# Performance work log

Hardware: AMD Instinct MI355X
Metric: run time of the kernel (lower is better)

The kernel has to match this reference:

```python
import jax, jax.numpy as jnp
import numpy as np

B, K, F, HID, NCLS = 32, 32, 2048, 2, 47
BN_EPS = 1e-5


def setup_inputs() -> dict:
    key = jax.random.key(0)
    ks = jax.random.split(key, 12)
    x = jax.random.normal(ks[0], (B, 1, F), dtype=jnp.float32)
    neighbor = jax.random.normal(ks[1], (B, K, 1, F), dtype=jnp.float32)
    # FeatBrd1d conv1d kernel_size=1 weights: (out_ch, in_ch)
    w1 = jax.random.normal(ks[2], (HID, 1), dtype=jnp.float32) * 0.5
    b1 = jax.random.normal(ks[3], (HID,), dtype=jnp.float32) * 0.1
    g1 = jnp.ones((HID,), dtype=jnp.float32)
    beta1 = jnp.zeros((HID,), dtype=jnp.float32)
    w2 = jax.random.normal(ks[4], (HID, HID), dtype=jnp.float32) * 0.5
    b2 = jax.random.normal(ks[5], (HID,), dtype=jnp.float32) * 0.1
    g2 = jnp.ones((HID,), dtype=jnp.float32)
    beta2 = jnp.zeros((HID,), dtype=jnp.float32)
    Wc = jax.random.normal(ks[6], (NCLS, HID * F), dtype=jnp.float32) * (1.0 / np.sqrt(HID * F))
    bc = jnp.zeros((NCLS,), dtype=jnp.float32)
    return {"x": x, "neighbor": neighbor, "w1": w1, "b1": b1, "g1": g1,
            "beta1": beta1, "w2": w2, "b2": b2, "g2": g2, "beta2": beta2,
            "Wc": Wc, "bc": bc}


def feature_adjacency(x, neighbor):
    # fadj[b] = sum_{k} x[b,0,:] outer neighbor[b,k,0,:]  -> (B, F, F)
    ysum = neighbor.sum(axis=(1, 2))                      # (B, F)
    fadj = jnp.einsum('bf,bg->bfg', x[:, 0, :], ysum)
    fadj = fadj + jnp.swapaxes(fadj, -2, -1)
    # sgnroot
    fadj = jnp.sign(fadj) * jnp.sqrt(jnp.abs(fadj))
    # row_normalize (torch sums over dim=1 of (B,F,F))
    denom = jnp.abs(fadj).sum(axis=1, keepdims=True) + 1e-7
    fadj = fadj / denom
    return jnp.nan_to_num(fadj, nan=0.0, posinf=None, neginf=None)


def featbrd(x, fadj, w, b):
    # conv1d kernel-size-1: (B, Cin, F) x (Cout, Cin) -> (B, Cout, F)
    h = jnp.einsum('bif,oi->bof', x, w) + b[None, :, None]
    # adj broadcast: out[b,c,f] = sum_g fadj[b,f,g] * h[b,c,g]
    return jnp.einsum('bfg,bcg->bcf', fadj, h)


def bn_softsign(x, gamma, beta):
    # BatchNorm1d training mode over (B, C, F): stats per channel over (B, F)
    mean = x.mean(axis=(0, 2), keepdims=True)
    var = ((x - mean) ** 2).mean(axis=(0, 2), keepdims=True)
    xn = (x - mean) * jax.lax.rsqrt(var + BN_EPS)
    y = gamma[None, :, None] * xn + beta[None, :, None]
    return y / (1.0 + jnp.abs(y))  # Softsign


def reference(x, neighbor, w1, b1, g1, beta1, w2, b2, g2, beta2, Wc, bc):
    fadj = feature_adjacency(x, neighbor)
    h = bn_softsign(featbrd(x, fadj, w1, b1), g1, beta1)
    h = bn_softsign(featbrd(h, fadj, w2, b2), g2, beta2)
    flat = h.reshape(h.shape[0], -1)                      # (B, HID*F)
    return flat @ Wc.T + bc
```

## Files before the change

kernel.cpp:

```cpp
#include <hip/hip_runtime.h>
#include <math.h>

namespace {

constexpr int Bn   = 32;
constexpr int Kn   = 32;
constexpr int Fn   = 2048;
constexpr int HIDn = 2;
constexpr int NCLSn = 47;
constexpr float EPSn = 1e-5f;
constexpr int NT = 256;
constexpr int GS = 16;
constexpr int FT = Fn / GS;

typedef float v2f __attribute__((ext_vector_type(2)));
typedef float v4f __attribute__((ext_vector_type(4)));

__device__ inline float wave_sum(float v) {
    #pragma unroll
    for (int off = 32; off > 0; off >>= 1) v += __shfl_down(v, off, 64);
    return v;
}

__global__ void ysum_kernel(const float* __restrict__ neighbor,
                            float* __restrict__ ysum,
                            double* __restrict__ stats) {
    int idx4 = blockIdx.x * NT + threadIdx.x;
    if (blockIdx.x == 0 && threadIdx.x < 8) stats[threadIdx.x] = 0.0;
    int b = idx4 >> 9;
    int gq = idx4 & 511;
    const float* p = neighbor + (size_t)b * Kn * Fn + gq * 4;
    v4f s = (v4f){0.f, 0.f, 0.f, 0.f};
    #pragma unroll
    for (int k = 0; k < Kn; ++k) s += *(const v4f*)(p + (size_t)k * Fn);
    *(v4f*)(ysum + (size_t)b * Fn + gq * 4) = s;
}

__global__ __launch_bounds__(NT, 4)
void denom_partial_kernel(const float* __restrict__ x, const float* __restrict__ ysum,
                          float* __restrict__ dpart) {
    __shared__ v4f xyf4[FT];
    const int gtile = blockIdx.x;
    const int fs    = blockIdx.y;
    const int b     = blockIdx.z;
    const int tid   = threadIdx.x;
    const float* xb = x + (size_t)b * Fn;
    const float* yb = ysum + (size_t)b * Fn;
    if (tid < FT) {
        int f = fs * FT + tid;
        float xv = xb[f], yv = yb[f];
        xyf4[tid] = (v4f){xv, xv, yv, yv};
    }
    const int gbase = (gtile * NT + tid) * 4;
    const v4f Xg4 = *(const v4f*)(xb + gbase);
    const v4f Yg4 = *(const v4f*)(yb + gbase);
    const v2f Xg01 = (v2f){Xg4.x, Xg4.y}, Xg23 = (v2f){Xg4.z, Xg4.w};
    const v2f Yg01 = (v2f){Yg4.x, Yg4.y}, Yg23 = (v2f){Yg4.z, Yg4.w};
    __syncthreads();
    v2f d01 = (v2f){0.f, 0.f}, d23 = (v2f){0.f, 0.f};
    #pragma unroll 8
    for (int j = 0; j < FT; ++j) {
        v4f q = xyf4[j];
        v2f xf = (v2f){q.x, q.y}, yf = (v2f){q.z, q.w};
        v2f vA = Xg01 * yf + Yg01 * xf;
        v2f vB = Xg23 * yf + Yg23 * xf;
        v2f sA, sB;
        sA.x = __builtin_amdgcn_sqrtf(fabsf(vA.x));
        sA.y = __builtin_amdgcn_sqrtf(fabsf(vA.y));
        sB.x = __builtin_amdgcn_sqrtf(fabsf(vB.x));
        sB.y = __builtin_amdgcn_sqrtf(fabsf(vB.y));
        d01 += sA;
        d23 += sB;
    }
    v4f dout = (v4f){d01.x, d01.y, d23.x, d23.y};
    *(v4f*)(dpart + ((size_t)fs * Bn + b) * Fn + gbase) = dout;
}

__device__ inline void mv_loop4(const v4f* __restrict__ xy4, const v4f* __restrict__ tt4,
                                v2f Xf01, v2f Xf23, v2f Yf01, v2f Yf23,
                                v2f& a00, v2f& a10, v2f& a01, v2f& a11) {
    #pragma unroll 8
    for (int j = 0; j < FT; ++j) {
        v4f q = xy4[j];
        v2f xg = (v2f){q.x, q.y}, yg = (v2f){q.z, q.w};
        v2f vA = Xf01 * yg + Yf01 * xg;
        v2f vB = Xf23 * yg + Yf23 * xg;
        v2f SA, SB;
        SA.x = copysignf(__builtin_amdgcn_sqrtf(fabsf(vA.x)), vA.x);
        SA.y = copysignf(__builtin_amdgcn_sqrtf(fabsf(vA.y)), vA.y);
        SB.x = copysignf(__builtin_amdgcn_sqrtf(fabsf(vB.x)), vB.x);
        SB.y = copysignf(__builtin_amdgcn_sqrtf(fabsf(vB.y)), vB.y);
        v4f u = tt4[j];
        v2f t0 = (v2f){u.x, u.y}, t1 = (v2f){u.z, u.w};
        a00 += SA * t0;
        a10 += SA * t1;
        a01 += SB * t0;
        a11 += SB * t1;
    }
}

__global__ __launch_bounds__(NT, 4)
void mv1_partial_kernel(const float* __restrict__ x, const float* __restrict__ ysum,
                        const float* __restrict__ dpart,
                        const float* __restrict__ w1, const float* __restrict__ b1,
                        float* __restrict__ part) {
    __shared__ v4f xy4[FT], tt4[FT];
    const int ftile = blockIdx.x;
    const int gs    = blockIdx.y;
    const int b     = blockIdx.z;
    const int tid   = threadIdx.x;
    const float* xb = x + (size_t)b * Fn;
    const float* yb = ysum + (size_t)b * Fn;
    if (tid < FT) {
        int g = gs * FT + tid;
        float d = 0.f;
        #pragma unroll
        for (int fs = 0; fs < GS; ++fs) d += dpart[((size_t)fs * Bn + b) * Fn + g];
        float r = 1.0f / (d + 1e-7f);
        float xg = xb[g], yg = yb[g];
        float t0 = fmaf(w1[0], xg, b1[0]) * r;
        float t1 = fmaf(w1[1], xg, b1[1]) * r;
        xy4[tid] = (v4f){xg, xg, yg, yg};
        tt4[tid] = (v4f){t0, t0, t1, t1};
    }
    const int fbase = (ftile * NT + tid) * 4;
    const v4f X4 = *(const v4f*)(xb + fbase);
    const v4f Y4 = *(const v4f*)(yb + fbase);
    __syncthreads();
    v2f a00 = (v2f){0.f, 0.f}, a10 = a00, a01 = a00, a11 = a00;
    mv_loop4(xy4, tt4,
             (v2f){X4.x, X4.y}, (v2f){X4.z, X4.w},
             (v2f){Y4.x, Y4.y}, (v2f){Y4.z, Y4.w}, a00, a10, a01, a11);
    size_t base = (((size_t)gs * Bn + b) * HIDn) * Fn;
    *(v4f*)(part + base + fbase)      = (v4f){a00.x, a00.y, a01.x, a01.y};
    *(v4f*)(part + base + Fn + fbase) = (v4f){a10.x, a10.y, a11.x, a11.y};
}

__global__ __launch_bounds__(NT, 4)
void mv2_partial_kernel(const float* __restrict__ x, const float* __restrict__ ysum,
                        const float* __restrict__ dpart, const float* __restrict__ out1,
                        const double* __restrict__ stats,
                        const float* __restrict__ g1, const float* __restrict__ beta1,
                        const float* __restrict__ w2, const float* __restrict__ b2,
                        float* __restrict__ part) {
    __shared__ v4f xy4[FT], tt4[FT];
    const int ftile = blockIdx.x;
    const int gs    = blockIdx.y;
    const int b     = blockIdx.z;
    const int tid   = threadIdx.x;
    const float* xb = x + (size_t)b * Fn;
    const float* yb = ysum + (size_t)b * Fn;
    if (tid < FT) {
        const double N = (double)(Bn * Fn);
        double m0d = stats[0] / N, m1d = stats[1] / N;
        float mean0 = (float)m0d, mean1 = (float)m1d;
        float var0 = (float)(stats[2] / N - m0d * m0d);
        float var1 = (float)(stats[3] / N - m1d * m1d);
        float inv0 = rsqrtf(var0 + EPSn) * g1[0];
        float inv1 = rsqrtf(var1 + EPSn) * g1[1];
        int g = gs * FT + tid;
        float d = 0.f;
        #pragma unroll
        for (int fs = 0; fs < GS; ++fs) d += dpart[((size_t)fs * Bn + b) * Fn + g];
        float r = 1.0f / (d + 1e-7f);
        size_t obase = ((size_t)b * HIDn) * Fn + g;
        float o0 = out1[obase], o1 = out1[obase + Fn];
        float y0 = fmaf(o0 - mean0, inv0, beta1[0]);
        float y1 = fmaf(o1 - mean1, inv1, beta1[1]);
        float z0 = y0 / (1.f + fabsf(y0));
        float z1 = y1 / (1.f + fabsf(y1));
        float t0 = fmaf(w2[0], z0, fmaf(w2[1], z1, b2[0])) * r;
        float t1 = fmaf(w2[2], z0, fmaf(w2[3], z1, b2[1])) * r;
        float xg = xb[g], yg = yb[g];
        xy4[tid] = (v4f){xg, xg, yg, yg};
        tt4[tid] = (v4f){t0, t0, t1, t1};
    }
    const int fbase = (ftile * NT + tid) * 4;
    const v4f X4 = *(const v4f*)(xb + fbase);
    const v4f Y4 = *(const v4f*)(yb + fbase);
    __syncthreads();
    v2f a00 = (v2f){0.f, 0.f}, a10 = a00, a01 = a00, a11 = a00;
    mv_loop4(xy4, tt4,
             (v2f){X4.x, X4.y}, (v2f){X4.z, X4.w},
             (v2f){Y4.x, Y4.y}, (v2f){Y4.z, Y4.w}, a00, a10, a01, a11);
    size_t base = (((size_t)gs * Bn + b) * HIDn) * Fn;
    *(v4f*)(part + base + fbase)      = (v4f){a00.x, a00.y, a01.x, a01.y};
    *(v4f*)(part + base + Fn + fbase) = (v4f){a10.x, a10.y, a11.x, a11.y};
}

__global__ void mv_reduce_kernel(const float* __restrict__ part, float* __restrict__ out,
                                 double* __restrict__ stats) {
    __shared__ float red[4][4];
    int pidx = blockIdx.x * NT + threadIdx.x;
    int b = pidx >> 9;
    int fq = pidx & 511;
    const size_t stride = (size_t)Bn * HIDn * Fn;
    size_t base = ((size_t)b * HIDn) * Fn + fq * 4;
    v4f o0 = (v4f){0.f, 0.f, 0.f, 0.f}, o1 = o0;
    #pragma unroll
    for (int gs = 0; gs < GS; ++gs) {
        o0 += *(const v4f*)(part + (size_t)gs * stride + base);
        o1 += *(const v4f*)(part + (size_t)gs * stride + base + Fn);
    }
    *(v4f*)(out + base)      = o0;
    *(v4f*)(out + base + Fn) = o1;
    float s0 = wave_sum((o0.x + o0.y) + (o0.z + o0.w));
    float s1 = wave_sum((o1.x + o1.y) + (o1.z + o1.w));
    float q0 = wave_sum((o0.x * o0.x + o0.y * o0.y) + (o0.z * o0.z + o0.w * o0.w));
    float q1 = wave_sum((o1.x * o1.x + o1.y * o1.y) + (o1.z * o1.z + o1.w * o1.w));
    int wid = threadIdx.x >> 6, lane = threadIdx.x & 63;
    if (lane == 0) { red[wid][0] = s0; red[wid][1] = s1; red[wid][2] = q0; red[wid][3] = q1; }
    __syncthreads();
    if (threadIdx.x == 0) {
        double S0 = 0, S1 = 0, Q0 = 0, Q1 = 0;
        #pragma unroll
        for (int w = 0; w < 4; ++w) {
            S0 += red[w][0]; S1 += red[w][1]; Q0 += red[w][2]; Q1 += red[w][3];
        }
        atomicAdd(&stats[0], S0);
        atomicAdd(&stats[1], S1);
        atomicAdd(&stats[2], Q0);
        atomicAdd(&stats[3], Q1);
    }
}

__global__ void classifier_kernel(const float* __restrict__ out2, const double* __restrict__ stats,
                                  const float* __restrict__ g2, const float* __restrict__ beta2,
                                  const float* __restrict__ Wc, const float* __restrict__ bc,
                                  float* __restrict__ out) {
    __shared__ float z[HIDn * Fn];
    const int n = blockIdx.x;
    const int b = blockIdx.y;
    const double N = (double)(Bn * Fn);
    double m0d = stats[0] / N, m1d = stats[1] / N;
    float mean0 = (float)m0d, mean1 = (float)m1d;
    float var0 = (float)(stats[2] / N - m0d * m0d);
    float var1 = (float)(stats[3] / N - m1d * m1d);
    float inv0 = rsqrtf(var0 + EPSn) * g2[0];
    float inv1 = rsqrtf(var1 + EPSn) * g2[1];
    float bet0 = beta2[0], bet1 = beta2[1];
    const float* src = out2 + (size_t)b * HIDn * Fn;
    #pragma unroll
    for (int it = 0; it < (HIDn * Fn) / NT; ++it) {
        int i = it * NT + threadIdx.x;
        int c = i >> 11;
        float v = src[i];
        float y = fmaf(v - (c ? mean1 : mean0), (c ? inv1 : inv0), (c ? bet1 : bet0));
        z[i] = y / (1.f + fabsf(y));
    }
    __syncthreads();
    const float4* z4 = (const float4*)z;
    const float4* w4 = (const float4*)(Wc + (size_t)n * (HIDn * Fn));
    float acc = 0.f;
    #pragma unroll
    for (int it = 0; it < (HIDn * Fn) / (4 * NT); ++it) {
        int i = it * NT + threadIdx.x;
        float4 a = z4[i];
        float4 w = w4[i];
        acc = fmaf(a.x, w.x, acc);
        acc = fmaf(a.y, w.y, acc);
        acc = fmaf(a.z, w.z, acc);
        acc = fmaf(a.w, w.w, acc);
    }
    __shared__ float red[4];
    float s = wave_sum(acc);
    int wid = threadIdx.x >> 6, lane = threadIdx.x & 63;
    if (lane == 0) red[wid] = s;
    __syncthreads();
    if (threadIdx.x == 0) {
        float tot = (red[0] + red[1]) + (red[2] + red[3]);
        out[(size_t)b * NCLSn + n] = tot + bc[n];
    }
}

}

extern "C" void kernel_launch(void* const* d_in, const int* in_sizes, int n_in,
                              void* d_out, int out_size, void* d_ws, size_t ws_size,
                              hipStream_t stream) {
    const float* x        = (const float*)d_in[0];
    const float* neighbor = (const float*)d_in[1];
    const float* w1       = (const float*)d_in[2];
    const float* b1       = (const float*)d_in[3];
    const float* g1       = (const float*)d_in[4];
    const float* beta1    = (const float*)d_in[5];
    const float* w2       = (const float*)d_in[6];
    const float* b2       = (const float*)d_in[7];
    const float* g2       = (const float*)d_in[8];
    const float* beta2    = (const float*)d_in[9];
    const float* Wc       = (const float*)d_in[10];
    const float* bc       = (const float*)d_in[11];
    float* out = (float*)d_out;

    float* ws    = (float*)d_ws;
    float* ysum  = ws;
    float* dpart = ysum + Bn * Fn;
    float* part  = dpart + (size_t)GS * Bn * Fn;
    float* out1  = part + (size_t)GS * Bn * HIDn * Fn;
    float* out2  = out1 + Bn * HIDn * Fn;
    double* stats = (double*)(out2 + Bn * HIDn * Fn);

    const dim3 grid_split(Fn / (NT * 4), GS, Bn);

    ysum_kernel<<<(Bn * Fn / 4) / NT, NT, 0, stream>>>(neighbor, ysum, stats);
    denom_partial_kernel<<<grid_split, NT, 0, stream>>>(x, ysum, dpart);
    mv1_partial_kernel<<<grid_split, NT, 0, stream>>>(x, ysum, dpart, w1, b1, part);
    mv_reduce_kernel<<<(Bn * Fn / 4) / NT, NT, 0, stream>>>(part, out1, stats);
    mv2_partial_kernel<<<grid_split, NT, 0, stream>>>(x, ysum, dpart, out1, stats, g1, beta1, w2, b2, part);
    mv_reduce_kernel<<<(Bn * Fn / 4) / NT, NT, 0, stream>>>(part, out2, stats + 4);
    classifier_kernel<<<dim3(NCLSn, Bn), NT, 0, stream>>>(out2, stats + 4, g2, beta2, Wc, bc, out);
}
```

Before: 92.96 us.

## Widen per-thread tiles to 8 columns, double split count, cache reciprocal denominators

```diff
diff --git a/kernel.cpp b/kernel.cpp
--- a/kernel.cpp
+++ b/kernel.cpp
@@ -10,7 +10,7 @@
 constexpr int NCLSn = 47;
 constexpr float EPSn = 1e-5f;
 constexpr int NT = 256;
-constexpr int GS = 16;
+constexpr int GS = 32;
 constexpr int FT = Fn / GS;
 
 typedef float v2f __attribute__((ext_vector_type(2)));
@@ -40,10 +40,9 @@
 void denom_partial_kernel(const float* __restrict__ x, const float* __restrict__ ysum,
                           float* __restrict__ dpart) {
     __shared__ v4f xyf4[FT];
-    const int gtile = blockIdx.x;
-    const int fs    = blockIdx.y;
-    const int b     = blockIdx.z;
-    const int tid   = threadIdx.x;
+    const int fs  = blockIdx.x;
+    const int b   = blockIdx.y;
+    const int tid = threadIdx.x;
     const float* xb = x + (size_t)b * Fn;
     const float* yb = ysum + (size_t)b * Fn;
     if (tid < FT) {
@@ -51,51 +50,49 @@
         float xv = xb[f], yv = yb[f];
         xyf4[tid] = (v4f){xv, xv, yv, yv};
     }
-    const int gbase = (gtile * NT + tid) * 4;
-    const v4f Xg4 = *(const v4f*)(xb + gbase);
-    const v4f Yg4 = *(const v4f*)(yb + gbase);
-    const v2f Xg01 = (v2f){Xg4.x, Xg4.y}, Xg23 = (v2f){Xg4.z, Xg4.w};
-    const v2f Yg01 = (v2f){Yg4.x, Yg4.y}, Yg23 = (v2f){Yg4.z, Yg4.w};
-    __syncthreads();
-    v2f d01 = (v2f){0.f, 0.f}, d23 = (v2f){0.f, 0.f};
+    const int gbase = tid * 8;
+    const v4f Xa = *(const v4f*)(xb + gbase);
+    const v4f Xb = *(const v4f*)(xb + gbase + 4);
+    const v4f Ya = *(const v4f*)(yb + gbase);
+    const v4f Yb = *(const v4f*)(yb + gbase + 4);
+    v2f Xg[4] = {(v2f){Xa.x, Xa.y}, (v2f){Xa.z, Xa.w}, (v2f){Xb.x, Xb.y}, (v2f){Xb.z, Xb.w}};
+    v2f Yg[4] = {(v2f){Ya.x, Ya.y}, (v2f){Ya.z, Ya.w}, (v2f){Yb.x, Yb.y}, (v2f){Yb.z, Yb.w}};
+    __syncthreads();
+    v2f d[4] = {(v2f){0.f, 0.f}, (v2f){0.f, 0.f}, (v2f){0.f, 0.f}, (v2f){0.f, 0.f}};
     #pragma unroll 8
     for (int j = 0; j < FT; ++j) {
         v4f q = xyf4[j];
         v2f xf = (v2f){q.x, q.y}, yf = (v2f){q.z, q.w};
-        v2f vA = Xg01 * yf + Yg01 * xf;
-        v2f vB = Xg23 * yf + Yg23 * xf;
-        v2f sA, sB;
-        sA.x = __builtin_amdgcn_sqrtf(fabsf(vA.x));
-        sA.y = __builtin_amdgcn_sqrtf(fabsf(vA.y));
-        sB.x = __builtin_amdgcn_sqrtf(fabsf(vB.x));
-        sB.y = __builtin_amdgcn_sqrtf(fabsf(vB.y));
-        d01 += sA;
-        d23 += sB;
-    }
-    v4f dout = (v4f){d01.x, d01.y, d23.x, d23.y};
-    *(v4f*)(dpart + ((size_t)fs * Bn + b) * Fn + gbase) = dout;
-}
-
-__device__ inline void mv_loop4(const v4f* __restrict__ xy4, const v4f* __restrict__ tt4,
-                                v2f Xf01, v2f Xf23, v2f Yf01, v2f Yf23,
-                                v2f& a00, v2f& a10, v2f& a01, v2f& a11) {
+        #pragma unroll
+        for (int p = 0; p < 4; ++p) {
+            v2f v = Xg[p] * yf + Yg[p] * xf;
+            d[p].x += __builtin_amdgcn_sqrtf(fabsf(v.x));
+            d[p].y += __builtin_amdgcn_sqrtf(fabsf(v.y));
+        }
+    }
+    size_t base = ((size_t)fs * Bn + b) * Fn + gbase;
+    *(v4f*)(dpart + base)     = (v4f){d[0].x, d[0].y, d[1].x, d[1].y};
+    *(v4f*)(dpart + base + 4) = (v4f){d[2].x, d[2].y, d[3].x, d[3].y};
+}
+
+__device__ inline void mv_loop8(const v4f* __restrict__ xy4, const v4f* __restrict__ tt4,
+                                const v2f Xf[4], const v2f Yf[4],
+                                v2f a0[4], v2f a1[4]) {
     #pragma unroll 8
     for (int j = 0; j < FT; ++j) {
         v4f q = xy4[j];
         v2f xg = (v2f){q.x, q.y}, yg = (v2f){q.z, q.w};
-        v2f vA = Xf01 * yg + Yf01 * xg;
-        v2f vB = Xf23 * yg + Yf23 * xg;
-        v2f SA, SB;
-        SA.x = copysignf(__builtin_amdgcn_sqrtf(fabsf(vA.x)), vA.x);
-        SA.y = copysignf(__builtin_amdgcn_sqrtf(fabsf(vA.y)), vA.y);
-        SB.x = copysignf(__builtin_amdgcn_sqrtf(fabsf(vB.x)), vB.x);
-        SB.y = copysignf(__builtin_amdgcn_sqrtf(fabsf(vB.y)), vB.y);
         v4f u = tt4[j];
         v2f t0 = (v2f){u.x, u.y}, t1 = (v2f){u.z, u.w};
-        a00 += SA * t0;
-        a10 += SA * t1;
-        a01 += SB * t0;
-        a11 += SB * t1;
+        #pragma unroll
+        for (int p = 0; p < 4; ++p) {
+            v2f v = Xf[p] * yg + Yf[p] * xg;
+            v2f S;
+            S.x = copysignf(__builtin_amdgcn_sqrtf(fabsf(v.x)), v.x);
+            S.y = copysignf(__builtin_amdgcn_sqrtf(fabsf(v.y)), v.y);
+            a0[p] += S * t0;
+            a1[p] += S * t1;
+        }
     }
 }
 
@@ -103,51 +100,66 @@
 void mv1_partial_kernel(const float* __restrict__ x, const float* __restrict__ ysum,
                         const float* __restrict__ dpart,
                         const float* __restrict__ w1, const float* __restrict__ b1,
-                        float* __restrict__ part) {
+                        float* __restrict__ rden, float* __restrict__ part) {
     __shared__ v4f xy4[FT], tt4[FT];
-    const int ftile = blockIdx.x;
-    const int gs    = blockIdx.y;
-    const int b     = blockIdx.z;
-    const int tid   = threadIdx.x;
+    __shared__ float redp[4][FT];
+    const int gs  = blockIdx.x;
+    const int b   = blockIdx.y;
+    const int tid = threadIdx.x;
     const float* xb = x + (size_t)b * Fn;
     const float* yb = ysum + (size_t)b * Fn;
+    {
+        int grp = tid >> 6, gi = tid & 63;
+        int g = gs * FT + gi;
+        float p = 0.f;
+        #pragma unroll
+        for (int k = 0; k < GS / 4; ++k) {
+            int fs = grp * (GS / 4) + k;
+            p += dpart[((size_t)fs * Bn + b) * Fn + g];
+        }
+        redp[grp][gi] = p;
+    }
+    __syncthreads();
     if (tid < FT) {
         int g = gs * FT + tid;
-        float d = 0.f;
-        #pragma unroll
-        for (int fs = 0; fs < GS; ++fs) d += dpart[((size_t)fs * Bn + b) * Fn + g];
+        float d = (redp[0][tid] + redp[1][tid]) + (redp[2][tid] + redp[3][tid]);
         float r = 1.0f / (d + 1e-7f);
+        rden[(size_t)b * Fn + g] = r;
         float xg = xb[g], yg = yb[g];
         float t0 = fmaf(w1[0], xg, b1[0]) * r;
         float t1 = fmaf(w1[1], xg, b1[1]) * r;
         xy4[tid] = (v4f){xg, xg, yg, yg};
         tt4[tid] = (v4f){t0, t0, t1, t1};
     }
-    const int fbase = (ftile * NT + tid) * 4;
-    const v4f X4 = *(const v4f*)(xb + fbase);
-    const v4f Y4 = *(const v4f*)(yb + fbase);
-    __syncthreads();
-    v2f a00 = (v2f){0.f, 0.f}, a10 = a00, a01 = a00, a11 = a00;
-    mv_loop4(xy4, tt4,
-             (v2f){X4.x, X4.y}, (v2f){X4.z, X4.w},
-             (v2f){Y4.x, Y4.y}, (v2f){Y4.z, Y4.w}, a00, a10, a01, a11);
+    const int fbase = tid * 8;
+    const v4f Xa = *(const v4f*)(xb + fbase);
+    const v4f Xb = *(const v4f*)(xb + fbase + 4);
+    const v4f Ya = *(const v4f*)(yb + fbase);
+    const v4f Yb = *(const v4f*)(yb + fbase + 4);
+    v2f Xf[4] = {(v2f){Xa.x, Xa.y}, (v2f){Xa.z, Xa.w}, (v2f){Xb.x, Xb.y}, (v2f){Xb.z, Xb.w}};
+    v2f Yf[4] = {(v2f){Ya.x, Ya.y}, (v2f){Ya.z, Ya.w}, (v2f){Yb.x, Yb.y}, (v2f){Yb.z, Yb.w}};
+    __syncthreads();
+    v2f a0[4] = {(v2f){0.f, 0.f}, (v2f){0.f, 0.f}, (v2f){0.f, 0.f}, (v2f){0.f, 0.f}};
+    v2f a1[4] = {(v2f){0.f, 0.f}, (v2f){0.f, 0.f}, (v2f){0.f, 0.f}, (v2f){0.f, 0.f}};
+    mv_loop8(xy4, tt4, Xf, Yf, a0, a1);
     size_t base = (((size_t)gs * Bn + b) * HIDn) * Fn;
-    *(v4f*)(part + base + fbase)      = (v4f){a00.x, a00.y, a01.x, a01.y};
-    *(v4f*)(part + base + Fn + fbase) = (v4f){a10.x, a10.y, a11.x, a11.y};
+    *(v4f*)(part + base + fbase)          = (v4f){a0[0].x, a0[0].y, a0[1].x, a0[1].y};
+    *(v4f*)(part + base + fbase + 4)      = (v4f){a0[2].x, a0[2].y, a0[3].x, a0[3].y};
+    *(v4f*)(part + base + Fn + fbase)     = (v4f){a1[0].x, a1[0].y, a1[1].x, a1[1].y};
+    *(v4f*)(part + base + Fn + fbase + 4) = (v4f){a1[2].x, a1[2].y, a1[3].x, a1[3].y};
 }
 
 __global__ __launch_bounds__(NT, 4)
 void mv2_partial_kernel(const float* __restrict__ x, const float* __restrict__ ysum,
-                        const float* __restrict__ dpart, const float* __restrict__ out1,
+                        const float* __restrict__ rden, const float* __restrict__ out1,
                         const double* __restrict__ stats,
                         const float* __restrict__ g1, const float* __restrict__ beta1,
                         const float* __restrict__ w2, const float* __restrict__ b2,
                         float* __restrict__ part) {
     __shared__ v4f xy4[FT], tt4[FT];
-    const int ftile = blockIdx.x;
-    const int gs    = blockIdx.y;
-    const int b     = blockIdx.z;
-    const int tid   = threadIdx.x;
+    const int gs  = blockIdx.x;
+    const int b   = blockIdx.y;
+    const int tid = threadIdx.x;
     const float* xb = x + (size_t)b * Fn;
     const float* yb = ysum + (size_t)b * Fn;
     if (tid < FT) {
@@ -159,10 +171,7 @@
         float inv0 = rsqrtf(var0 + EPSn) * g1[0];
         float inv1 = rsqrtf(var1 + EPSn) * g1[1];
         int g = gs * FT + tid;
-        float d = 0.f;
-        #pragma unroll
-        for (int fs = 0; fs < GS; ++fs) d += dpart[((size_t)fs * Bn + b) * Fn + g];
-        float r = 1.0f / (d + 1e-7f);
+        float r = rden[(size_t)b * Fn + g];
         size_t obase = ((size_t)b * HIDn) * Fn + g;
         float o0 = out1[obase], o1 = out1[obase + Fn];
         float y0 = fmaf(o0 - mean0, inv0, beta1[0]);
@@ -175,17 +184,22 @@
         xy4[tid] = (v4f){xg, xg, yg, yg};
         tt4[tid] = (v4f){t0, t0, t1, t1};
     }
-    const int fbase = (ftile * NT + tid) * 4;
-    const v4f X4 = *(const v4f*)(xb + fbase);
-    const v4f Y4 = *(const v4f*)(yb + fbase);
-    __syncthreads();
-    v2f a00 = (v2f){0.f, 0.f}, a10 = a00, a01 = a00, a11 = a00;
-    mv_loop4(xy4, tt4,
-             (v2f){X4.x, X4.y}, (v2f){X4.z, X4.w},
-             (v2f){Y4.x, Y4.y}, (v2f){Y4.z, Y4.w}, a00, a10, a01, a11);
+    const int fbase = tid * 8;
+    const v4f Xa = *(const v4f*)(xb + fbase);
+    const v4f Xb = *(const v4f*)(xb + fbase + 4);
+    const v4f Ya = *(const v4f*)(yb + fbase);
+    const v4f Yb = *(const v4f*)(yb + fbase + 4);
+    v2f Xf[4] = {(v2f){Xa.x, Xa.y}, (v2f){Xa.z, Xa.w}, (v2f){Xb.x, Xb.y}, (v2f){Xb.z, Xb.w}};
+    v2f Yf[4] = {(v2f){Ya.x, Ya.y}, (v2f){Ya.z, Ya.w}, (v2f){Yb.x, Yb.y}, (v2f){Yb.z, Yb.w}};
+    __syncthreads();
+    v2f a0[4] = {(v2f){0.f, 0.f}, (v2f){0.f, 0.f}, (v2f){0.f, 0.f}, (v2f){0.f, 0.f}};
+    v2f a1[4] = {(v2f){0.f, 0.f}, (v2f){0.f, 0.f}, (v2f){0.f, 0.f}, (v2f){0.f, 0.f}};
+    mv_loop8(xy4, tt4, Xf, Yf, a0, a1);
     size_t base = (((size_t)gs * Bn + b) * HIDn) * Fn;
-    *(v4f*)(part + base + fbase)      = (v4f){a00.x, a00.y, a01.x, a01.y};
-    *(v4f*)(part + base + Fn + fbase) = (v4f){a10.x, a10.y, a11.x, a11.y};
+    *(v4f*)(part + base + fbase)          = (v4f){a0[0].x, a0[0].y, a0[1].x, a0[1].y};
+    *(v4f*)(part + base + fbase + 4)      = (v4f){a0[2].x, a0[2].y, a0[3].x, a0[3].y};
+    *(v4f*)(part + base + Fn + fbase)     = (v4f){a1[0].x, a1[0].y, a1[1].x, a1[1].y};
+    *(v4f*)(part + base + Fn + fbase + 4) = (v4f){a1[2].x, a1[2].y, a1[3].x, a1[3].y};
 }
 
 __global__ void mv_reduce_kernel(const float* __restrict__ part, float* __restrict__ out,
@@ -294,19 +308,20 @@
 
     float* ws    = (float*)d_ws;
     float* ysum  = ws;
-    float* dpart = ysum + Bn * Fn;
+    float* rden  = ysum + Bn * Fn;
+    float* dpart = rden + Bn * Fn;
     float* part  = dpart + (size_t)GS * Bn * Fn;
     float* out1  = part + (size_t)GS * Bn * HIDn * Fn;
     float* out2  = out1 + Bn * HIDn * Fn;
     double* stats = (double*)(out2 + Bn * HIDn * Fn);
 
-    const dim3 grid_split(Fn / (NT * 4), GS, Bn);
+    const dim3 grid_split(GS, Bn);
 
     ysum_kernel<<<(Bn * Fn / 4) / NT, NT, 0, stream>>>(neighbor, ysum, stats);
     denom_partial_kernel<<<grid_split, NT, 0, stream>>>(x, ysum, dpart);
-    mv1_partial_kernel<<<grid_split, NT, 0, stream>>>(x, ysum, dpart, w1, b1, part);
+    mv1_partial_kernel<<<grid_split, NT, 0, stream>>>(x, ysum, dpart, w1, b1, rden, part);
     mv_reduce_kernel<<<(Bn * Fn / 4) / NT, NT, 0, stream>>>(part, out1, stats);
-    mv2_partial_kernel<<<grid_split, NT, 0, stream>>>(x, ysum, dpart, out1, stats, g1, beta1, w2, b2, part);
+    mv2_partial_kernel<<<grid_split, NT, 0, stream>>>(x, ysum, rden, out1, stats, g1, beta1, w2, b2, part);
     mv_reduce_kernel<<<(Bn * Fn / 4) / NT, NT, 0, stream>>>(part, out2, stats + 4);
     classifier_kernel<<<dim3(NCLSn, Bn), NT, 0, stream>>>(out2, stats + 4, g2, beta2, Wc, bc, out);
 }
```

Result: slower. 100.2 us (+7.8%).
